# Kernel tuning notes

Hardware: AMD Instinct MI355X
Metric: run time of the kernel (lower is better)

The kernel has to match this reference:

```python
import jax, jax.numpy as jnp
import numpy as np

B, T, D, N = 2, 2048, 1024, 16
H = D // N  # 64

def setup_inputs() -> dict:
    key = jax.random.key(0)
    ks = jax.random.split(key, 5)
    s = 0.02
    return {
        "x": jax.random.normal(ks[0], (B, T, D), dtype=jnp.float32),
        "w_attn": jax.random.normal(ks[1], (D, 3 * D), dtype=jnp.float32) * s,
        "b_attn": jax.random.normal(ks[2], (3 * D,), dtype=jnp.float32) * s,
        "w_proj": jax.random.normal(ks[3], (D, D), dtype=jnp.float32) * s,
        "b_proj": jax.random.normal(ks[4], (D,), dtype=jnp.float32) * s,
    }

def reference(x, w_attn, b_attn, w_proj, b_proj):
    # qkv projection: (B,T,3D)
    qkv = jnp.einsum('btd,de->bte', x, w_attn) + b_attn
    q, k, v = jnp.split(qkv, 3, axis=-1)
    q = q.reshape(B, T, N, H)
    k = k.reshape(B, T, N, H)
    v = v.reshape(B, T, N, H)
    scale = jnp.asarray(H ** 0.5, dtype=x.dtype)
    # scores: (B, T_q, T_kv, N) -- matches torch einsum 'btnh,bsnh->btsn'
    scores = jnp.einsum('btnh,bsnh->btsn', q, k) / scale
    # causal mask, past_len = 0 (no kv cache)
    causal = jnp.tril(jnp.ones((T, T), dtype=bool))  # (T_q, T_kv)
    scores = jnp.where(causal[None, :, :, None], scores, jnp.asarray(-jnp.inf, dtype=scores.dtype))
    weights = jax.nn.softmax(scores, axis=2)  # softmax over kv axis
    out = jnp.einsum('btsn,bsnh->btnh', weights, v).reshape(B, T, D)
    output = jnp.einsum('btd,de->bte', out, w_proj) + b_proj
    return output, k, v
```

## Files before the change

### kernel.cpp

```cpp
#include <hip/hip_runtime.h>
#include <hip/hip_bf16.h>


typedef __attribute__((ext_vector_type(8))) short bf16x8;
typedef __attribute__((ext_vector_type(4))) float f32x4;

#define MFMA16(a, b, c) __builtin_amdgcn_mfma_f32_16x16x32_bf16(a, b, c, 0, 0, 0)

static constexpr int Bb = 2, Tt = 2048, Dd = 1024, Nn = 16, Hh = 64;
static constexpr float NEG_BIG = -30000.0f;
static constexpr float QSCALE  = 0.125f;

__device__ __forceinline__ short f2bf(float f) {
    __hip_bfloat16 h = __float2bfloat16(f);
    short s; __builtin_memcpy(&s, &h, 2); return s;
}
__device__ __forceinline__ float bf2f(short s) {
    __hip_bfloat16 h; __builtin_memcpy(&h, &s, 2); return __bfloat162float(h);
}
__device__ __forceinline__ bf16x8 cvt8(const float* __restrict__ p) {
    f32x4 a = *(const f32x4*)p, b = *(const f32x4*)(p + 4);
    bf16x8 r;
    #pragma unroll
    for (int j = 0; j < 4; ++j) { r[j] = f2bf(a[j]); r[4 + j] = f2bf(b[j]); }
    return r;
}
__device__ __forceinline__ bf16x8 cvt8s(const float* __restrict__ p, float s) {
    f32x4 a = *(const f32x4*)p, b = *(const f32x4*)(p + 4);
    bf16x8 r;
    #pragma unroll
    for (int j = 0; j < 4; ++j) { r[j] = f2bf(a[j] * s); r[4 + j] = f2bf(b[j] * s); }
    return r;
}

__device__ __forceinline__ void gload16(const short* g, short* l) {
    __builtin_amdgcn_global_load_lds(
        (const __attribute__((address_space(1))) unsigned int*)g,
        (__attribute__((address_space(3))) unsigned int*)l, 16, 0, 0);
}

template<int CTRL>
__device__ __forceinline__ float dppf(float x) {
    int i; __builtin_memcpy(&i, &x, 4);
    i = __builtin_amdgcn_update_dpp(0, i, CTRL, 0xf, 0xf, true);
    float r; __builtin_memcpy(&r, &i, 4); return r;
}
__device__ __forceinline__ float rowmax16(float x) {
    x = fmaxf(x, dppf<0x128>(x)); x = fmaxf(x, dppf<0x124>(x));
    x = fmaxf(x, dppf<0x122>(x)); x = fmaxf(x, dppf<0x121>(x));
    return x;
}
__device__ __forceinline__ float rowsum16(float x) {
    x += dppf<0x128>(x); x += dppf<0x124>(x);
    x += dppf<0x122>(x); x += dppf<0x121>(x);
    return x;
}

__global__ __launch_bounds__(256) void prep(
    const float* __restrict__ x, const float* __restrict__ wa,
    const float* __restrict__ wp,
    short* __restrict__ xb, short* __restrict__ wat, short* __restrict__ wpt)
{
    const int bid = blockIdx.x, tid = threadIdx.x;
    if (bid < 1024) {
        __shared__ float s[64][65];
        const float* src; short* dst; int Nc, k0, n0;
        if (bid < 768) { src = wa; dst = wat; Nc = 3072; k0 = (bid & 15) * 64; n0 = (bid >> 4) * 64; }
        else { int b2 = bid - 768; src = wp; dst = wpt; Nc = 1024; k0 = (b2 & 15) * 64; n0 = (b2 >> 4) * 64; }
        const int row = tid >> 2, cg = (tid & 3) * 16;
        const float* p = src + (size_t)(k0 + row) * Nc + n0 + cg;
        #pragma unroll
        for (int i = 0; i < 4; ++i) {
            f32x4 v = *(const f32x4*)(p + 4 * i);
            #pragma unroll
            for (int j = 0; j < 4; ++j) s[row][cg + 4 * i + j] = v[j];
        }
        __syncthreads();
        bf16x8 o0, o1;
        #pragma unroll
        for (int j = 0; j < 8; ++j) { o0[j] = f2bf(s[cg + j][row]); o1[j] = f2bf(s[cg + 8 + j][row]); }
        short* q = dst + (size_t)(n0 + row) * 1024 + k0 + cg;
        *(bf16x8*)q = o0; *(bf16x8*)(q + 8) = o1;
    } else {
        const size_t base = (size_t)(bid - 1024) * 2048 + tid * 8;
        *(bf16x8*)(xb + base) = cvt8(x + base);
    }
}

template<int MODE>
__global__ __launch_bounds__(256) void gemm128(
    const short* __restrict__ A, const short* __restrict__ Bt,
    const float* __restrict__ bias,
    float* __restrict__ fk, float* __restrict__ fv,
    short* __restrict__ qb, short* __restrict__ kb, short* __restrict__ vt,
    float* __restrict__ fout, int K)
{
    __shared__ short sA[2][128][32];
    __shared__ short sB[2][128][32];
    const int tid = threadIdx.x, lane = tid & 63, wave = tid >> 6;
    const int l15 = lane & 15, quad = lane >> 4;
    const int m0 = blockIdx.x * 128, n0 = blockIdx.y * 128;
    const int wr = (wave >> 1) * 64, wc = (wave & 1) * 64;

    const int rl  = lane >> 2;
    const int csh = (lane & 3) * 8;
    const size_t aOff0 = (size_t)(m0 + wave * 16 + rl) * K + csh;
    const size_t aOff1 = aOff0 + (size_t)64 * K;
    const size_t bOff0 = (size_t)(n0 + wave * 16 + rl) * K + csh;
    const size_t bOff1 = bOff0 + (size_t)64 * K;

    f32x4 acc[4][4] = {};

#define STAGE_G(pp, kk)                                            \
    do {                                                           \
        gload16(A  + aOff0 + (kk), &sA[pp][wave * 16][0]);         \
        gload16(A  + aOff1 + (kk), &sA[pp][64 + wave * 16][0]);    \
        gload16(Bt + bOff0 + (kk), &sB[pp][wave * 16][0]);         \
        gload16(Bt + bOff1 + (kk), &sB[pp][64 + wave * 16][0]);    \
    } while (0)

    STAGE_G(0, 0);
    int p = 0;
    for (int k0 = 0; k0 < K; k0 += 32, p ^= 1) {
        __syncthreads();
        if (k0 + 32 < K) STAGE_G(p ^ 1, k0 + 32);
        bf16x8 af[4], bfr[4];
        #pragma unroll
        for (int mt = 0; mt < 4; ++mt) af[mt]  = *(const bf16x8*)&sA[p][wr + mt * 16 + l15][quad * 8];
        #pragma unroll
        for (int nt = 0; nt < 4; ++nt) bfr[nt] = *(const bf16x8*)&sB[p][wc + nt * 16 + l15][quad * 8];
        #pragma unroll
        for (int mt = 0; mt < 4; ++mt)
        #pragma unroll
        for (int nt = 0; nt < 4; ++nt)
            acc[mt][nt] = MFMA16(af[mt], bfr[nt], acc[mt][nt]);
    }
#undef STAGE_G

    #pragma unroll
    for (int mt = 0; mt < 4; ++mt)
    #pragma unroll
    for (int nt = 0; nt < 4; ++nt) {
        const int gc = n0 + wc + nt * 16 + l15;
        const float bv = bias[gc];
        #pragma unroll
        for (int r = 0; r < 4; ++r) {
            const int grow = m0 + wr + mt * 16 + quad * 4 + r;
            const float val = acc[mt][nt][r] + bv;
            if (MODE == 1) {
                const int reg = gc >> 10, c = gc & 1023;
                if (reg == 0) {
                    qb[(size_t)grow * 1024 + c] = f2bf(val * QSCALE);
                } else {
                    const int bidx = grow >> 11, tt = grow & 2047;
                    const int nh = c >> 6, h = c & 63;
                    if (reg == 1) {
                        fk[(size_t)grow * 1024 + c] = val;
                        kb[((size_t)(bidx * Nn + nh) * Tt + tt) * Hh + h] = f2bf(val);
                    } else {
                        fv[(size_t)grow * 1024 + c] = val;
                        vt[((size_t)(bidx * Nn + nh) * Hh + h) * Tt + tt] = f2bf(val);
                    }
                }
            } else {
                fout[(size_t)grow * 1024 + gc] = val;
            }
        }
    }
}

__global__ __launch_bounds__(512, 6) void attn5(
    const short* __restrict__ Qb, const short* __restrict__ Kb,
    const short* __restrict__ Vt,
    short* __restrict__ op_part, float* __restrict__ ls_part)
{
    const int by = 15 - (int)blockIdx.y;
    const int c  = blockIdx.z;
    if (c && by < 8) return;

    __shared__ short sK[2][64][64];
    __shared__ short sV[2][64][64];
    __shared__ short sP[8][16][72];

    const int tid = threadIdx.x, lane = tid & 63, wave = tid >> 6;
    const int l15 = lane & 15, quad = lane >> 4;
    const int head = blockIdx.x;
    const int b = head >> 4, n = head & 15;
    const int q0w = by * 128 + wave * 16;

    const int gmask = (q0w + 15) >> 6;
    const int g0 = c * 16;
    const int ntmax = min(16, 2 * by + 2 - g0);

    const size_t kvhead = (size_t)head * Tt * Hh;
    const short* kbh = Kb + kvhead;
    const short* vth = Vt + kvhead;

    const short* qp = Qb + ((size_t)b * Tt + q0w + l15) * Dd + n * Hh + quad * 8;
    const bf16x8 qf0 = *(const bf16x8*)qp;
    const bf16x8 qf1 = *(const bf16x8*)(qp + 32);

    const int sr   = wave * 8 + (lane >> 3);
    const int srcb = (((lane & 7) ^ (lane >> 3))) * 8;
    const int swz  = l15 & 7;
    const int bsw  = quad ^ swz;

    f32x4 o_acc[4] = {};
    float lsum[4] = {};

#define STAGE_KV(bb, ktb)                                               \
    do {                                                                \
        gload16(kbh + (size_t)((ktb) + sr) * Hh + srcb, &sK[bb][wave * 8][0]); \
        gload16(vth + (size_t)sr * Tt + (ktb) + srcb,   &sV[bb][wave * 8][0]); \
    } while (0)

    STAGE_KV(0, g0 * 64);
    __syncthreads();

    int buf = 0;
    for (int it = 0; it < ntmax; ++it) {
        const int kt = (g0 + it) * 64;
        if (it + 1 < ntmax) STAGE_KV(buf ^ 1, kt + 64);

        f32x4 s[4] = {};
        #pragma unroll
        for (int jp = 0; jp < 2; ++jp) {
            bf16x8 ka0 = *(const bf16x8*)&sK[buf][32 * jp      + l15][bsw * 8];
            bf16x8 kc0 = *(const bf16x8*)&sK[buf][32 * jp      + l15][(bsw ^ 4) * 8];
            bf16x8 ka1 = *(const bf16x8*)&sK[buf][32 * jp + 16 + l15][bsw * 8];
            bf16x8 kc1 = *(const bf16x8*)&sK[buf][32 * jp + 16 + l15][(bsw ^ 4) * 8];
            __builtin_amdgcn_s_setprio(1);
            s[2 * jp]     = MFMA16(qf0, ka0, s[2 * jp]);
            s[2 * jp]     = MFMA16(qf1, kc0, s[2 * jp]);
            s[2 * jp + 1] = MFMA16(qf0, ka1, s[2 * jp + 1]);
            s[2 * jp + 1] = MFMA16(qf1, kc1, s[2 * jp + 1]);
            __builtin_amdgcn_s_setprio(0);
        }

        const bool masked = (g0 + it >= gmask);
        #pragma unroll
        for (int r = 0; r < 4; ++r) {
            const int row = q0w + quad * 4 + r;
            float x0 = s[0][r], x1 = s[1][r], x2 = s[2][r], x3 = s[3][r];
            if (masked) {
                if (kt + l15      > row) x0 = NEG_BIG;
                if (kt + 16 + l15 > row) x1 = NEG_BIG;
                if (kt + 32 + l15 > row) x2 = NEG_BIG;
                if (kt + 48 + l15 > row) x3 = NEG_BIG;
            }
            const float p0 = __expf(x0), p1 = __expf(x1);
            const float p2 = __expf(x2), p3 = __expf(x3);
            lsum[r] += (p0 + p1) + (p2 + p3);
            short* pw = &sP[wave][quad * 4 + r][l15];
            pw[0] = f2bf(p0); pw[16] = f2bf(p1); pw[32] = f2bf(p2); pw[48] = f2bf(p3);
        }
        __asm__ volatile("s_waitcnt lgkmcnt(0)" ::: "memory");
        bf16x8 pf0 = *(const bf16x8*)&sP[wave][l15][quad * 8];
        bf16x8 pf1 = *(const bf16x8*)&sP[wave][l15][32 + quad * 8];
        #pragma unroll
        for (int hc = 0; hc < 4; ++hc) {
            bf16x8 v0 = *(const bf16x8*)&sV[buf][hc * 16 + l15][bsw * 8];
            bf16x8 v1 = *(const bf16x8*)&sV[buf][hc * 16 + l15][(bsw ^ 4) * 8];
            __builtin_amdgcn_s_setprio(1);
            o_acc[hc] = MFMA16(pf0, v0, o_acc[hc]);
            o_acc[hc] = MFMA16(pf1, v1, o_acc[hc]);
            __builtin_amdgcn_s_setprio(0);
        }
        __syncthreads();
        buf ^= 1;
    }
#undef STAGE_KV

    const int slot = head * 24 + (by < 8 ? by : 2 * by - 8 + c);
    short* opw = op_part + ((size_t)slot * 128 + wave * 16) * 64;
    #pragma unroll
    for (int r = 0; r < 4; ++r) {
        const float l = rowsum16(lsum[r]);
        const int rloc = quad * 4 + r;
        if (l15 == 0) ls_part[slot * 128 + wave * 16 + rloc] = l;
        #pragma unroll
        for (int hc = 0; hc < 4; ++hc)
            opw[rloc * 64 + hc * 16 + l15] = f2bf(o_acc[hc][r]);
    }
}

__global__ __launch_bounds__(256) void attn_reduce(
    const short* __restrict__ op_part, const float* __restrict__ ls_part,
    short* __restrict__ Ob)
{
    const int idx = blockIdx.x * 256 + threadIdx.x;
    const int r = idx >> 3;
    const int h0 = (idx & 7) * 8;
    const int head = r >> 11, t = r & 2047;
    const int by = t >> 7, tr = t & 127;
    const int nch = 1 + (by >= 8);
    const int base = head * 24 + (by < 8 ? by : 2 * by - 8);

    float acc[8] = {};
    float l = 0.f;
    for (int c = 0; c < nch; ++c) {
        const int slot = base + c;
        bf16x8 v = *(const bf16x8*)(op_part + ((size_t)slot * 128 + tr) * 64 + h0);
        #pragma unroll
        for (int j = 0; j < 8; ++j) acc[j] += bf2f(v[j]);
        l += ls_part[slot * 128 + tr];
    }
    const float rl = 1.0f / fmaxf(l, 1e-20f);
    bf16x8 o;
    #pragma unroll
    for (int j = 0; j < 8; ++j) o[j] = f2bf(acc[j] * rl);
    const int b = head >> 4, n = head & 15;
    *(bf16x8*)(Ob + ((size_t)(b * Tt + t)) * Dd + n * Hh + h0) = o;
}

__global__ __launch_bounds__(256) void gemm_bias_split(
    const float* __restrict__ A, const float* __restrict__ Bm,
    const float* __restrict__ bias,
    float* __restrict__ dst0, float* __restrict__ dst1, float* __restrict__ dst2,
    short* __restrict__ kb, short* __restrict__ vt,
    int K, int Ncols, int Dsplit)
{
    __shared__ short sA[64][40];
    __shared__ short sBt[64][40];
    const int tid  = threadIdx.x;
    const int lane = tid & 63;
    const int wave = tid >> 6;
    const int l15  = lane & 15;
    const int quad = lane >> 4;
    const int m0 = blockIdx.x * 64;
    const int n0 = blockIdx.y * 64;
    const int wm = (wave >> 1) * 32;
    const int wn = (wave & 1) * 32;
    const int ar = tid >> 2, ac = (tid & 3) * 8;
    const int bk = tid >> 3, bc = (tid & 7) * 8;

    f32x4 acc[2][2] = {};
    for (int k0 = 0; k0 < K; k0 += 32) {
        bf16x8 av = cvt8(A  + (size_t)(m0 + ar) * K     + k0 + ac);
        bf16x8 bv = cvt8(Bm + (size_t)(k0 + bk) * Ncols + n0 + bc);
        *(bf16x8*)&sA[ar][ac] = av;
        #pragma unroll
        for (int j = 0; j < 8; ++j) sBt[bc + j][bk] = bv[j];
        __syncthreads();
        bf16x8 a0 = *(const bf16x8*)&sA[wm + l15][quad * 8];
        bf16x8 a1 = *(const bf16x8*)&sA[wm + 16 + l15][quad * 8];
        bf16x8 b0 = *(const bf16x8*)&sBt[wn + l15][quad * 8];
        bf16x8 b1 = *(const bf16x8*)&sBt[wn + 16 + l15][quad * 8];
        acc[0][0] = MFMA16(a0, b0, acc[0][0]);
        acc[0][1] = MFMA16(a0, b1, acc[0][1]);
        acc[1][0] = MFMA16(a1, b0, acc[1][0]);
        acc[1][1] = MFMA16(a1, b1, acc[1][1]);
        __syncthreads();
    }
    #pragma unroll
    for (int i = 0; i < 2; ++i)
    #pragma unroll
    for (int j = 0; j < 2; ++j) {
        const int ncol = n0 + wn + j * 16 + l15;
        const float bvf = bias[ncol];
        float* dbase; int c, which;
        if (ncol < Dsplit)        { dbase = dst0; c = ncol;            which = 0; }
        else if (ncol < 2*Dsplit) { dbase = dst1; c = ncol - Dsplit;   which = 1; }
        else                      { dbase = dst2; c = ncol - 2*Dsplit; which = 2; }
        const int nh = c >> 6, h = c & 63;
        #pragma unroll
        for (int r = 0; r < 4; ++r) {
            const int mrow = m0 + wm + i * 16 + quad * 4 + r;
            const float val = acc[i][j][r] + bvf;
            dbase[(size_t)mrow * Dsplit + c] = val;
            if (which == 1 && kb) {
                const int bidx = mrow >> 11, tt = mrow & 2047;
                kb[((size_t)(bidx * Nn + nh) * Tt + tt) * Hh + h] = f2bf(val);
            } else if (which == 2 && vt) {
                const int bidx = mrow >> 11, tt = mrow & 2047;
                vt[((size_t)(bidx * Nn + nh) * Hh + h) * Tt + tt] = f2bf(val);
            }
        }
    }
}

__global__ __launch_bounds__(256) void attn_fast(
    const float* __restrict__ Q, const short* __restrict__ Kb,
    const short* __restrict__ Vt, float* __restrict__ O)
{
    __shared__ short sP[4][2][16][40];
    const int tid  = threadIdx.x;
    const int lane = tid & 63;
    const int wave = tid >> 6;
    const int l15  = lane & 15;
    const int quad = lane >> 4;
    const int b = blockIdx.x >> 4, n = blockIdx.x & 15;
    const int qg = ((int)gridDim.y - 1 - (int)blockIdx.y) * 4 + wave;
    const int q0 = qg * 16;

    const size_t ohead  = (size_t)b * Tt * Dd + (size_t)n * Hh;
    const size_t kvhead = (size_t)(b * Nn + n) * Tt * Hh;
    const short* kbh = Kb + kvhead;
    const short* vth = Vt + kvhead;

    const float* qrow = Q + ohead + (size_t)(q0 + l15) * Dd;
    const bf16x8 qf0 = cvt8s(qrow + quad * 8, QSCALE);
    const bf16x8 qf1 = cvt8s(qrow + 32 + quad * 8, QSCALE);

    float m_i[4], l_i[4];
    f32x4 o_acc[4] = {};
    #pragma unroll
    for (int r = 0; r < 4; ++r) { m_i[r] = NEG_BIG; l_i[r] = 0.f; }

    int par = 0;
    for (int kt = 0; kt < q0 + 16; kt += 32, par ^= 1) {
        f32x4 s0 = {}, s1 = {};
        {
            const short* k0 = kbh + (size_t)(kt + l15) * Hh + quad * 8;
            bf16x8 k0a = *(const bf16x8*)k0;
            bf16x8 k0b = *(const bf16x8*)(k0 + 32);
            const short* k1 = k0 + 16 * Hh;
            bf16x8 k1a = *(const bf16x8*)k1;
            bf16x8 k1b = *(const bf16x8*)(k1 + 32);
            s0 = MFMA16(qf0, k0a, s0); s0 = MFMA16(qf1, k0b, s0);
            s1 = MFMA16(qf0, k1a, s1); s1 = MFMA16(qf1, k1b, s1);
        }
        const int qr0 = q0 + quad * 4;
        #pragma unroll
        for (int r = 0; r < 4; ++r) {
            float x0 = (kt + l15      > qr0 + r) ? NEG_BIG : s0[r];
            float x1 = (kt + 16 + l15 > qr0 + r) ? NEG_BIG : s1[r];
            const float t  = rowmax16(fmaxf(x0, x1));
            const float mn = fmaxf(m_i[r], t);
            const float alpha = __expf(m_i[r] - mn);
            const float p0 = __expf(x0 - mn);
            const float p1 = __expf(x1 - mn);
            l_i[r] = l_i[r] * alpha + rowsum16(p0 + p1);
            m_i[r] = mn;
            #pragma unroll
            for (int hc = 0; hc < 4; ++hc) o_acc[hc][r] *= alpha;
            sP[wave][par][quad * 4 + r][l15]      = f2bf(p0);
            sP[wave][par][quad * 4 + r][16 + l15] = f2bf(p1);
        }
        __asm__ volatile("s_waitcnt lgkmcnt(0)" ::: "memory");
        bf16x8 pf = *(const bf16x8*)&sP[wave][par][l15][quad * 8];
        #pragma unroll
        for (int hc = 0; hc < 4; ++hc) {
            bf16x8 vf = *(const bf16x8*)(vth + (size_t)(hc * 16 + l15) * Tt + kt + quad * 8);
            o_acc[hc] = MFMA16(pf, vf, o_acc[hc]);
        }
    }
    #pragma unroll
    for (int r = 0; r < 4; ++r) {
        const float rl = 1.0f / fmaxf(l_i[r], 1e-20f);
        #pragma unroll
        for (int hc = 0; hc < 4; ++hc)
            O[ohead + (size_t)(q0 + quad * 4 + r) * Dd + hc * 16 + l15] = o_acc[hc][r] * rl;
    }
}

extern "C" void kernel_launch(void* const* d_in, const int* in_sizes, int n_in,
                              void* d_out, int out_size, void* d_ws, size_t ws_size,
                              hipStream_t stream) {
    const float* x      = (const float*)d_in[0];
    const float* w_attn = (const float*)d_in[1];
    const float* b_attn = (const float*)d_in[2];
    const float* w_proj = (const float*)d_in[3];
    const float* b_proj = (const float*)d_in[4];

    const size_t elems = (size_t)Bb * Tt * Dd;
    float* out  = (float*)d_out;
    float* kout = out  + elems;
    float* vout = kout + elems;

    const size_t NSLOT = (size_t)32 * 24;
    const size_t need_v2 = (4 * elems + (size_t)1024 * 1024 + NSLOT * 128 * 64) * 2
                         + NSLOT * 128 * 4;

    if (ws_size >= need_v2) {
        short* qb  = (short*)d_ws;
        short* kb  = qb + elems;
        short* vt  = kb + elems;
        short* wpt = vt + elems;
        short* xb  = wpt + (size_t)1024 * 1024;
        short* ob  = xb;
        short* op_part = xb + elems;
        float* ls_part = (float*)(op_part + NSLOT * 128 * 64);
        short* wat = op_part;

        prep<<<3072, 256, 0, stream>>>(x, w_attn, w_proj, xb, wat, wpt);
        gemm128<1><<<dim3(32, 24), 256, 0, stream>>>(
            xb, wat, b_attn, kout, vout, qb, kb, vt, nullptr, Dd);
        attn5<<<dim3(Bb * Nn, 16, 2), 512, 0, stream>>>(qb, kb, vt, op_part, ls_part);
        attn_reduce<<<2048, 256, 0, stream>>>(op_part, ls_part, ob);
        gemm128<2><<<dim3(32, 8), 256, 0, stream>>>(
            ob, wpt, b_proj, nullptr, nullptr, nullptr, nullptr, nullptr, out, Dd);
    } else {
        float* o_ws = (float*)d_ws;
        short* kb = (short*)((char*)d_ws + elems * 4);
        short* vt = kb + elems;
        gemm_bias_split<<<dim3((Bb * Tt) / 64, (3 * Dd) / 64), 256, 0, stream>>>(
            x, w_attn, b_attn, out, kout, vout, kb, vt, Dd, 3 * Dd, Dd);
        attn_fast<<<dim3(Bb * Nn, Tt / 64), 256, 0, stream>>>(out, kb, vt, o_ws);
        gemm_bias_split<<<dim3((Bb * Tt) / 64, Dd / 64), 256, 0, stream>>>(
            o_ws, w_proj, b_proj, out, out, out, nullptr, nullptr, Dd, Dd, Dd);
    }
}
```

Before: 215.6 us.

## Triple-buffer GEMM LDS pipeline and remap blocks to XCD-local tiles

The 128x128 bf16 GEMM moves from a double-buffered to a triple-buffered LDS pipeline. Loads are issued two stages ahead, and explicit vmcnt waits plus a raw s_barrier replace __syncthreads, so global-load latency overlaps more MFMA work. Block IDs are also remapped so the blocks landing on each XCD cover a contiguous M×N tile region, improving L2 reuse of A and B. The cost is 50% more LDS per block, which may lower occupancy, and the mapping hardcodes the grid shapes (32×24 and 32×8 tiles).

Result: faster. 202.2 us (-6.2%).

```diff
diff --git a/kernel.cpp b/kernel.cpp
--- a/kernel.cpp
+++ b/kernel.cpp
@@ -95,11 +95,18 @@
     short* __restrict__ qb, short* __restrict__ kb, short* __restrict__ vt,
     float* __restrict__ fout, int K)
 {
-    __shared__ short sA[2][128][32];
-    __shared__ short sB[2][128][32];
+    __shared__ short sA[3][128][32];
+    __shared__ short sB[3][128][32];
     const int tid = threadIdx.x, lane = tid & 63, wave = tid >> 6;
     const int l15 = lane & 15, quad = lane >> 4;
-    const int m0 = blockIdx.x * 128, n0 = blockIdx.y * 128;
+
+    const int lid = (int)blockIdx.y * (int)gridDim.x + (int)blockIdx.x;
+    const int xcd = lid & 7, sidx = lid >> 3;
+    constexpr int SN = (MODE == 1) ? 12 : 4;
+    const int mt = (xcd & 3) * 8 + (sidx & 7);
+    const int ntl = (xcd >> 2) * SN + (sidx >> 3);
+    const int m0 = mt * 128, n0 = ntl * 128;
+
     const int wr = (wave >> 1) * 64, wc = (wave & 1) * 64;
 
     const int rl  = lane >> 2;
@@ -120,33 +127,46 @@
     } while (0)
 
     STAGE_G(0, 0);
-    int p = 0;
-    for (int k0 = 0; k0 < K; k0 += 32, p ^= 1) {
-        __syncthreads();
-        if (k0 + 32 < K) STAGE_G(p ^ 1, k0 + 32);
+    STAGE_G(1, 32);
+
+    int cur = 0;
+    for (int k0 = 0; k0 < K; k0 += 32) {
+        if (k0 + 32 < K) {
+            asm volatile("s_waitcnt vmcnt(4)" ::: "memory");
+        } else {
+            asm volatile("s_waitcnt vmcnt(0)" ::: "memory");
+        }
+        __builtin_amdgcn_s_barrier();
+        __builtin_amdgcn_sched_barrier(0);
+
+        const int nxt2 = cur >= 1 ? cur - 1 : cur + 2;
+        if (k0 + 64 < K) STAGE_G(nxt2, k0 + 64);
+
         bf16x8 af[4], bfr[4];
         #pragma unroll
-        for (int mt = 0; mt < 4; ++mt) af[mt]  = *(const bf16x8*)&sA[p][wr + mt * 16 + l15][quad * 8];
-        #pragma unroll
-        for (int nt = 0; nt < 4; ++nt) bfr[nt] = *(const bf16x8*)&sB[p][wc + nt * 16 + l15][quad * 8];
-        #pragma unroll
-        for (int mt = 0; mt < 4; ++mt)
-        #pragma unroll
-        for (int nt = 0; nt < 4; ++nt)
-            acc[mt][nt] = MFMA16(af[mt], bfr[nt], acc[mt][nt]);
+        for (int mt2 = 0; mt2 < 4; ++mt2) af[mt2]  = *(const bf16x8*)&sA[cur][wr + mt2 * 16 + l15][quad * 8];
+        #pragma unroll
+        for (int nt2 = 0; nt2 < 4; ++nt2) bfr[nt2] = *(const bf16x8*)&sB[cur][wc + nt2 * 16 + l15][quad * 8];
+        #pragma unroll
+        for (int mt2 = 0; mt2 < 4; ++mt2)
+        #pragma unroll
+        for (int nt2 = 0; nt2 < 4; ++nt2)
+            acc[mt2][nt2] = MFMA16(af[mt2], bfr[nt2], acc[mt2][nt2]);
+
+        cur = cur < 2 ? cur + 1 : 0;
     }
 #undef STAGE_G
 
     #pragma unroll
-    for (int mt = 0; mt < 4; ++mt)
-    #pragma unroll
-    for (int nt = 0; nt < 4; ++nt) {
-        const int gc = n0 + wc + nt * 16 + l15;
+    for (int mt2 = 0; mt2 < 4; ++mt2)
+    #pragma unroll
+    for (int nt2 = 0; nt2 < 4; ++nt2) {
+        const int gc = n0 + wc + nt2 * 16 + l15;
         const float bv = bias[gc];
         #pragma unroll
         for (int r = 0; r < 4; ++r) {
-            const int grow = m0 + wr + mt * 16 + quad * 4 + r;
-            const float val = acc[mt][nt][r] + bv;
+            const int grow = m0 + wr + mt2 * 16 + quad * 4 + r;
+            const float val = acc[mt2][nt2][r] + bv;
             if (MODE == 1) {
                 const int reg = gc >> 10, c = gc & 1023;
                 if (reg == 0) {
```
